# Kernel tuning notes

Measured on AMD Instinct MI355X. Metric: run time of the kernel, lower is better.

The kernel has to match this reference:

```python
import jax, jax.numpy as jnp
import numpy as np

N_WIN = 7    # n_win hardcoded in AR_Attention
TOPK = 4     # topk routing windows
HEADS = 8    # num_heads


def setup_inputs() -> dict:
    key = jax.random.key(0)
    ks = jax.random.split(key, 6)
    B, H, W, C = 4, 56, 56, 256
    s = 0.02
    x = jax.random.normal(ks[0], (B, H, W, C), jnp.float32)
    Wqkv = jax.random.normal(ks[1], (C, 3 * C), jnp.float32) * s  # Linear(dim, 3*dim) (qk_dim=dim)
    bqkv = jnp.zeros((3 * C,), jnp.float32)
    Wo = jax.random.normal(ks[2], (C, C), jnp.float32) * s        # output projection Linear(dim, dim)
    bo = jnp.zeros((C,), jnp.float32)
    lepe_w = jax.random.normal(ks[3], (5, 5, 1, C), jnp.float32) * s  # 5x5 depthwise conv (side_dwconv=5)
    lepe_b = jnp.zeros((C,), jnp.float32)
    return {"x": x, "Wqkv": Wqkv, "bqkv": bqkv, "Wo": Wo, "bo": bo,
            "lepe_w": lepe_w, "lepe_b": lepe_b}


def reference(x, Wqkv, bqkv, Wo, bo, lepe_w, lepe_b):
    B, H, W, C = x.shape
    nw = N_WIN
    h, w = H // nw, W // nw           # region size (8x8)
    p2 = nw * nw                      # number of regions (49)
    hd = C // HEADS                   # head dim
    scale = float(C) ** -0.5          # qk_scale = qk_dim ** -0.5 (qk_dim = dim)

    # region partition: [B,H,W,C] -> [B,p2,h,w,C]
    xr = x.reshape(B, nw, h, nw, w, C).transpose(0, 1, 3, 2, 4, 5).reshape(B, p2, h, w, C)

    qkv = xr @ Wqkv + bqkv            # [B,p2,h,w,3C]
    q, kv = qkv[..., :C], qkv[..., C:]

    q_pix = q.reshape(B, p2, h * w, C)
    kv_pix = kv.reshape(B, p2, h * w, 2 * C)   # kv_downsample_mode='identity'

    # region-level queries/keys via per-window mean pooling
    q_win = q.mean((2, 3))                     # [B,p2,C]
    k_win = kv[..., :C].mean((2, 3))           # [B,p2,C]

    # LEPE: 5x5 depthwise conv on v over the full image grid
    v_img = kv[..., C:].reshape(B, nw, nw, h, w, C).transpose(0, 1, 3, 2, 4, 5).reshape(B, H, W, C)
    lepe = jax.lax.conv_general_dilated(
        v_img, lepe_w, (1, 1), 'SAME',
        dimension_numbers=('NHWC', 'HWIO', 'NHWC'),
        feature_group_count=C) + lepe_b

    # top-k window routing (param_routing=False, hard routing, mul_weight='none')
    r_logit = jnp.einsum('bpc,bqc->bpq', q_win * scale, k_win)  # [B,p2,p2]
    _, r_idx = jax.lax.top_k(r_logit, TOPK)                     # [B,p2,TOPK]

    # gather selected kv windows: [B,p2,TOPK,h*w,2C]
    kv_sel = jax.vmap(lambda kvp, i: kvp[i])(kv_pix, r_idx)

    k_sel = kv_sel[..., :C].reshape(B, p2, TOPK * h * w, HEADS, hd)
    v_sel = kv_sel[..., C:].reshape(B, p2, TOPK * h * w, HEADS, hd)
    qh = q_pix.reshape(B, p2, h * w, HEADS, hd)

    attn = jnp.einsum('bpqnd,bpknd->bpnqk', qh * scale, k_sel)  # [B,p2,heads,hw,TOPK*hw]
    attn = jax.nn.softmax(attn, axis=-1)
    out = jnp.einsum('bpnqk,bpknd->bpqnd', attn, v_sel).reshape(B, p2, h, w, C)

    # windows back to image grid
    out = out.reshape(B, nw, nw, h, w, C).transpose(0, 1, 3, 2, 4, 5).reshape(B, H, W, C)
    out = out + lepe
    return out @ Wo + bo
```

## Files before the change

kernel.cpp:

```cpp
#include <hip/hip_runtime.h>
#include <hip/hip_bf16.h>

#define NPIX 12544

typedef short bf16x8 __attribute__((ext_vector_type(8)));
typedef float f32x4  __attribute__((ext_vector_type(4)));

__device__ __forceinline__ float bf2f(unsigned short u) {
    unsigned int x = ((unsigned int)u) << 16;
    float f; __builtin_memcpy(&f, &x, sizeof(f)); return f;
}
__device__ __forceinline__ unsigned short f2bf(float f) {
    __hip_bfloat16 h = __float2bfloat16(f);
    unsigned short u; __builtin_memcpy(&u, &h, 2); return u;
}
__device__ __forceinline__ void load_lds16(const unsigned short* g, unsigned short* l) {
    __builtin_amdgcn_global_load_lds(
        (const __attribute__((address_space(1))) unsigned int*)g,
        (__attribute__((address_space(3))) unsigned int*)l,
        16, 0, 0);
}

__global__ __launch_bounds__(256) void k_prep(
    const float* __restrict__ X, unsigned short* __restrict__ Xb,
    float* __restrict__ xmean,
    const float* __restrict__ Wqkv, const float* __restrict__ Wo,
    unsigned short* __restrict__ Wtq, unsigned short* __restrict__ Wto)
{
    __shared__ __align__(16) unsigned char sm[64 * 65 * 4];
    const int t = threadIdx.x;
    const int blk = blockIdx.x;
    if (blk < 392) {
        float* part = (float*)sm;
        const int w = blk >> 1, hc = blk & 1;
        const int b = w / 49, p = w % 49;
        const int wi = p / 7, wj = p % 7;
        const int ch0 = hc * 128;
        const int ps = t >> 5, cg = t & 31;
        float4 s = {0.f, 0.f, 0.f, 0.f};
        #pragma unroll
        for (int i = 0; i < 8; i++) {
            int pp = ps * 8 + i;
            int y = wi * 8 + (pp >> 3), x = wj * 8 + (pp & 7);
            int idx = (((b * 56) + y) * 56 + x) * 256 + ch0 + cg * 4;
            float4 v = *reinterpret_cast<const float4*>(X + idx);
            s.x += v.x; s.y += v.y; s.z += v.z; s.w += v.w;
            ushort4 o = { f2bf(v.x), f2bf(v.y), f2bf(v.z), f2bf(v.w) };
            *reinterpret_cast<ushort4*>(Xb + idx) = o;
        }
        *reinterpret_cast<float4*>(part + t * 4) = *reinterpret_cast<float4*>(&s);
        __syncthreads();
        if (t < 32) {
            float4 m = {0.f, 0.f, 0.f, 0.f};
            #pragma unroll
            for (int ps2 = 0; ps2 < 8; ps2++) {
                float4 v = *reinterpret_cast<float4*>(part + (ps2 * 32 + t) * 4);
                m.x += v.x; m.y += v.y; m.z += v.z; m.w += v.w;
            }
            m.x *= (1.f / 64.f); m.y *= (1.f / 64.f);
            m.z *= (1.f / 64.f); m.w *= (1.f / 64.f);
            *reinterpret_cast<float4*>(xmean + w * 256 + ch0 + t * 4) = m;
        }
    } else {
        float* tile = (float*)sm;
        int tb = blk - 392;
        const float* Wsrc; unsigned short* Wdst; int N, kt, nt;
        if (tb < 48) { Wsrc = Wqkv; Wdst = Wtq; N = 768; kt = tb / 12; nt = tb % 12; }
        else { tb -= 48; Wsrc = Wo; Wdst = Wto; N = 256; kt = tb / 4; nt = tb % 4; }
        const int k0 = kt * 64, n0 = nt * 64;
        const int r0 = t >> 6, c = t & 63;
        #pragma unroll
        for (int i = 0; i < 16; i++) {
            int r = i * 4 + r0;
            tile[r * 65 + c] = Wsrc[(size_t)(k0 + r) * N + n0 + c];
        }
        __syncthreads();
        #pragma unroll
        for (int i = 0; i < 16; i++) {
            int n = i * 4 + r0;
            Wdst[(size_t)(n0 + n) * 256 + k0 + c] = f2bf(tile[c * 65 + n]);
        }
    }
}

__global__ __launch_bounds__(256) void k_main1(
    const unsigned short* __restrict__ A,
    const unsigned short* __restrict__ Bt,
    const float* __restrict__ bias,
    unsigned short* __restrict__ O,
    const float* __restrict__ xmean,
    const float* __restrict__ Wqkv,
    float* __restrict__ qwin, float* __restrict__ kwin)
{
    __shared__ __align__(16) unsigned char sm1[16384];
    const int t = threadIdx.x;
    const int blk = blockIdx.x;
    if (blk < 588) {
        unsigned short* As = (unsigned short*)sm1;
        unsigned short* Bs = (unsigned short*)(sm1 + 8192);
        const int m0 = (blk % 98) * 128, n0 = (blk / 98) * 128;
        const int wave = t >> 6, lane = t & 63, quad = lane >> 4, lo = lane & 15;
        const int wm = wave & 1, wn = wave >> 1;
        const int sr = wave * 16 + (lane >> 2);
        const int sc = lane & 3;
        f32x4 acc[4][4];
        #pragma unroll
        for (int i = 0; i < 4; i++)
            #pragma unroll
            for (int j = 0; j < 4; j++) acc[i][j] = (f32x4){0.f, 0.f, 0.f, 0.f};

        for (int kt = 0; kt < 256; kt += 32) {
            __syncthreads();
            #pragma unroll
            for (int j = 0; j < 2; j++) {
                int row = j * 64 + sr;
                int e = sc ^ ((row >> 1) & 3);
                load_lds16(A  + (size_t)(m0 + row) * 256 + kt + e * 8, &As[row * 32 + sc * 8]);
                load_lds16(Bt + (size_t)(n0 + row) * 256 + kt + e * 8, &Bs[row * 32 + sc * 8]);
            }
            __syncthreads();
            bf16x8 af[4], bfr[4];
            #pragma unroll
            for (int mt = 0; mt < 4; mt++) {
                int row = wm * 64 + mt * 16 + lo;
                int c = quad ^ ((row >> 1) & 3);
                af[mt] = *reinterpret_cast<const bf16x8*>(&As[row * 32 + c * 8]);
            }
            #pragma unroll
            for (int nt = 0; nt < 4; nt++) {
                int col = wn * 64 + nt * 16 + lo;
                int c = quad ^ ((col >> 1) & 3);
                bfr[nt] = *reinterpret_cast<const bf16x8*>(&Bs[col * 32 + c * 8]);
            }
            #pragma unroll
            for (int mt = 0; mt < 4; mt++)
                #pragma unroll
                for (int nt = 0; nt < 4; nt++)
                    acc[mt][nt] = __builtin_amdgcn_mfma_f32_16x16x32_bf16(
                        af[mt], bfr[nt], acc[mt][nt], 0, 0, 0);
        }
        float bv[4];
        #pragma unroll
        for (int nt = 0; nt < 4; nt++) bv[nt] = bias[n0 + wn * 64 + nt * 16 + lo];
        #pragma unroll
        for (int mt = 0; mt < 4; mt++)
            #pragma unroll
            for (int nt = 0; nt < 4; nt++) {
                int n = n0 + wn * 64 + nt * 16 + lo;
                #pragma unroll
                for (int r = 0; r < 4; r++) {
                    int m = m0 + wm * 64 + mt * 16 + quad * 4 + r;
                    O[m * 768 + n] = f2bf(acc[mt][nt][r] + bv[nt]);
                }
            }
    } else {
        float* xs = (float*)sm1;
        const int u = blk - 588;
        const int bp = u % 196;
        const int half = u / 196;
        const int c = t;
        xs[c] = xmean[bp * 256 + c];
        __syncthreads();
        const int col = half * 256 + c;
        float a = 0.f;
        for (int k = 0; k < 256; k++) a += xs[k] * Wqkv[k * 768 + col];
        float* outp = half ? kwin : qwin;
        outp[bp * 256 + c] = a + bias[col];
    }
}

__global__ __launch_bounds__(256) void k_main2(
    const float* __restrict__ qwin, const float* __restrict__ kwin,
    int* __restrict__ ridx,
    const unsigned short* __restrict__ QKV,
    const float* __restrict__ lw, const float* __restrict__ lb,
    unsigned short* __restrict__ Olepe)
{
    __shared__ __align__(16) unsigned char sm2[25600];
    const int t = threadIdx.x;
    const int blk = blockIdx.x;
    if (blk < 196) {
        float* part = (float*)sm2;
        float* lg   = (float*)(sm2 + 49 * 4 * 4);
        const int b = blk / 49, p = blk % 49;
        if (t < 196) {
            int d = t >> 2, pr = t & 3;
            const float* qp = &qwin[(b * 49 + p) * 256];
            const float* kp = &kwin[(b * 49 + d) * 256];
            float a = 0.f;
            for (int ch = pr * 64; ch < pr * 64 + 64; ch++) a += qp[ch] * kp[ch];
            part[d * 4 + pr] = a;
        }
        __syncthreads();
        if (t < 49) lg[t] = part[t * 4 + 0] + part[t * 4 + 1] + part[t * 4 + 2] + part[t * 4 + 3];
        __syncthreads();
        if (t == 0) {
            unsigned long long used = 0ull;
            for (int sel = 0; sel < 4; sel++) {
                float best = -1e30f; int bi = 0;
                for (int qq = 0; qq < 49; qq++)
                    if (!((used >> qq) & 1ull) && lg[qq] > best) { best = lg[qq]; bi = qq; }
                used |= (1ull << bi);
                ridx[blk * 4 + sel] = bi;
            }
        }
    } else {
        float* lws = (float*)sm2;
        #pragma unroll
        for (int i = 0; i < 25; i++) lws[i * 256 + t] = lw[i * 256 + t];

        const int pl = t & 7;
        const int cg = t >> 3;
        const int c0 = cg * 8;
        const int gid = (blk - 196) * 8 + pl;
        const int b = gid / 3136, rem = gid % 3136;
        const int y = rem / 56, x = rem % 56;
        __syncthreads();

        float acc[8];
        {
            float4 b0 = *reinterpret_cast<const float4*>(lb + c0);
            float4 b1 = *reinterpret_cast<const float4*>(lb + c0 + 4);
            acc[0] = b0.x; acc[1] = b0.y; acc[2] = b0.z; acc[3] = b0.w;
            acc[4] = b1.x; acc[5] = b1.y; acc[6] = b1.z; acc[7] = b1.w;
        }
        #pragma unroll
        for (int ky = 0; ky < 5; ky++) {
            int yy = y + ky - 2;
            if (yy < 0 || yy >= 56) continue;
            #pragma unroll
            for (int kx = 0; kx < 5; kx++) {
                int xx = x + kx - 2;
                if (xx < 0 || xx >= 56) continue;
                bf16x8 v = *reinterpret_cast<const bf16x8*>(
                    QKV + (((b * 56) + yy) * 56 + xx) * 768 + 512 + c0);
                const float* wrow = &lws[(ky * 5 + kx) * 256 + c0];
                float4 w0 = *reinterpret_cast<const float4*>(wrow);
                float4 w1 = *reinterpret_cast<const float4*>(wrow + 4);
                acc[0] += bf2f((unsigned short)v[0]) * w0.x;
                acc[1] += bf2f((unsigned short)v[1]) * w0.y;
                acc[2] += bf2f((unsigned short)v[2]) * w0.z;
                acc[3] += bf2f((unsigned short)v[3]) * w0.w;
                acc[4] += bf2f((unsigned short)v[4]) * w1.x;
                acc[5] += bf2f((unsigned short)v[5]) * w1.y;
                acc[6] += bf2f((unsigned short)v[6]) * w1.z;
                acc[7] += bf2f((unsigned short)v[7]) * w1.w;
            }
        }
        bf16x8 o;
        #pragma unroll
        for (int j = 0; j < 8; j++) o[j] = (short)f2bf(acc[j]);
        *reinterpret_cast<bf16x8*>(Olepe + (size_t)gid * 256 + c0) = o;
    }
}

__global__ __launch_bounds__(256) void k_attn(
    const unsigned short* __restrict__ QKV,
    const int* __restrict__ ridx,
    const unsigned short* __restrict__ Olepe,
    unsigned short* __restrict__ Osum)
{
    __shared__ __align__(16) unsigned char smem[50688];
    unsigned short* Vt = (unsigned short*)smem;
    unsigned short* Qs = (unsigned short*)(smem + 16896);
    unsigned short* Ks = (unsigned short*)(smem + 22016);
    unsigned short* Ps = (unsigned short*)(smem + 16896);

    const int p = blockIdx.x, head = blockIdx.y, b = blockIdx.z;
    const int t = threadIdx.x;
    const int wi = p / 7, wj = p % 7;
    const int wave = t >> 6, lane = t & 63, quad = lane >> 4, lo = lane & 15;
    const int pix4 = t >> 2, c4 = t & 3;

    {
        int y = wi * 8 + (pix4 >> 3), x = wj * 8 + (pix4 & 7);
        const unsigned short* qp = QKV + (((b * 56) + y) * 56 + x) * 768 + head * 32 + c4 * 8;
        bf16x8 v = *reinterpret_cast<const bf16x8*>(qp);
        int sw = c4 ^ ((pix4 >> 3) & 3);
        *reinterpret_cast<bf16x8*>(&Qs[pix4 * 40 + sw * 8]) = v;
    }
    #pragma unroll
    for (int pass = 0; pass < 4; pass++) {
        int sel = ridx[(b * 49 + p) * 4 + pass];
        int si = sel / 7, sj = sel % 7;
        int y = si * 8 + (pix4 >> 3), x = sj * 8 + (pix4 & 7);
        const unsigned short* base = QKV + (((b * 56) + y) * 56 + x) * 768 + 256 + head * 32;
        bf16x8 kv = *reinterpret_cast<const bf16x8*>(base + c4 * 8);
        bf16x8 vv = *reinterpret_cast<const bf16x8*>(base + 256 + c4 * 8);
        int krow = pass * 64 + pix4;
        int sw = c4 ^ ((krow >> 3) & 3);
        *reinterpret_cast<bf16x8*>(&Ks[krow * 40 + sw * 8]) = kv;
        #pragma unroll
        for (int j = 0; j < 8; j++)
            Vt[(c4 * 8 + j) * 264 + krow] = (unsigned short)vv[j];
    }
    __syncthreads();

    f32x4 sc[16];
    {
        int row = wave * 16 + lo;
        bf16x8 af = *reinterpret_cast<const bf16x8*>(
            &Qs[row * 40 + ((quad ^ ((row >> 3) & 3)) * 8)]);
        f32x4 z = (f32x4){0.f, 0.f, 0.f, 0.f};
        #pragma unroll
        for (int nt = 0; nt < 16; nt++) {
            int key = nt * 16 + lo;
            bf16x8 bfr = *reinterpret_cast<const bf16x8*>(
                &Ks[key * 40 + ((quad ^ ((key >> 3) & 3)) * 8)]);
            sc[nt] = __builtin_amdgcn_mfma_f32_16x16x32_bf16(af, bfr, z, 0, 0, 0);
        }
    }
    float M[4] = {-1e30f, -1e30f, -1e30f, -1e30f};
    #pragma unroll
    for (int nt = 0; nt < 16; nt++)
        #pragma unroll
        for (int r = 0; r < 4; r++) M[r] = fmaxf(M[r], sc[nt][r] * 0.0625f);
    #pragma unroll
    for (int d = 1; d < 16; d <<= 1)
        #pragma unroll
        for (int r = 0; r < 4; r++) M[r] = fmaxf(M[r], __shfl_xor(M[r], d));
    float l[4] = {0.f, 0.f, 0.f, 0.f};
    #pragma unroll
    for (int nt = 0; nt < 16; nt++)
        #pragma unroll
        for (int r = 0; r < 4; r++) {
            float e = __expf(sc[nt][r] * 0.0625f - M[r]);
            sc[nt][r] = e;
            l[r] += e;
        }
    #pragma unroll
    for (int d = 1; d < 16; d <<= 1)
        #pragma unroll
        for (int r = 0; r < 4; r++) l[r] += __shfl_xor(l[r], d);

    __syncthreads();

    unsigned short* myPs = Ps + wave * 16 * 264;
    #pragma unroll
    for (int nt = 0; nt < 16; nt++)
        #pragma unroll
        for (int r = 0; r < 4; r++)
            myPs[(quad * 4 + r) * 264 + nt * 16 + lo] = f2bf(sc[nt][r]);

    f32x4 o0 = (f32x4){0.f, 0.f, 0.f, 0.f}, o1 = o0;
    #pragma unroll
    for (int kt = 0; kt < 8; kt++) {
        bf16x8 pa = *reinterpret_cast<const bf16x8*>(
            &myPs[lo * 264 + kt * 32 + quad * 8]);
        bf16x8 vb0 = *reinterpret_cast<const bf16x8*>(
            &Vt[lo * 264 + kt * 32 + quad * 8]);
        bf16x8 vb1 = *reinterpret_cast<const bf16x8*>(
            &Vt[(16 + lo) * 264 + kt * 32 + quad * 8]);
        o0 = __builtin_amdgcn_mfma_f32_16x16x32_bf16(pa, vb0, o0, 0, 0, 0);
        o1 = __builtin_amdgcn_mfma_f32_16x16x32_bf16(pa, vb1, o1, 0, 0, 0);
    }
    #pragma unroll
    for (int r = 0; r < 4; r++) {
        int q = wave * 16 + quad * 4 + r;
        int y = wi * 8 + (q >> 3), x = wj * 8 + (q & 7);
        size_t base = (size_t)(((b * 56) + y) * 56 + x) * 256 + head * 32;
        const unsigned short* lp = Olepe + base;
        unsigned short* op = Osum + base;
        float inv = 1.0f / l[r];
        op[lo]      = f2bf(o0[r] * inv + bf2f(lp[lo]));
        op[16 + lo] = f2bf(o1[r] * inv + bf2f(lp[16 + lo]));
    }
}

__global__ __launch_bounds__(256) void k_proj(
    const unsigned short* __restrict__ A,
    const unsigned short* __restrict__ Bt,
    const float* __restrict__ bias,
    float* __restrict__ O)
{
    __shared__ unsigned short As[128 * 32];
    __shared__ unsigned short Bs[64 * 32];
    const int t = threadIdx.x;
    const int m0 = blockIdx.x * 128, n0 = blockIdx.y * 64;
    const int wave = t >> 6, lane = t & 63, quad = lane >> 4, lo = lane & 15;
    const int sr = wave * 16 + (lane >> 2);
    const int sc = lane & 3;
    f32x4 acc[2][4];
    #pragma unroll
    for (int i = 0; i < 2; i++)
        #pragma unroll
        for (int j = 0; j < 4; j++) acc[i][j] = (f32x4){0.f, 0.f, 0.f, 0.f};

    for (int kt = 0; kt < 256; kt += 32) {
        __syncthreads();
        #pragma unroll
        for (int j = 0; j < 2; j++) {
            int row = j * 64 + sr;
            int e = sc ^ ((row >> 1) & 3);
            load_lds16(A + (size_t)(m0 + row) * 256 + kt + e * 8, &As[row * 32 + sc * 8]);
        }
        {
            int e = sc ^ ((sr >> 1) & 3);
            load_lds16(Bt + (size_t)(n0 + sr) * 256 + kt + e * 8, &Bs[sr * 32 + sc * 8]);
        }
        __syncthreads();
        bf16x8 af[2], bfr[4];
        #pragma unroll
        for (int mt = 0; mt < 2; mt++) {
            int row = wave * 32 + mt * 16 + lo;
            int c = quad ^ ((row >> 1) & 3);
            af[mt] = *reinterpret_cast<const bf16x8*>(&As[row * 32 + c * 8]);
        }
        #pragma unroll
        for (int nt = 0; nt < 4; nt++) {
            int col = nt * 16 + lo;
            int c = quad ^ ((col >> 1) & 3);
            bfr[nt] = *reinterpret_cast<const bf16x8*>(&Bs[col * 32 + c * 8]);
        }
        #pragma unroll
        for (int mt = 0; mt < 2; mt++)
            #pragma unroll
            for (int nt = 0; nt < 4; nt++)
                acc[mt][nt] = __builtin_amdgcn_mfma_f32_16x16x32_bf16(
                    af[mt], bfr[nt], acc[mt][nt], 0, 0, 0);
    }
    float bv[4];
    #pragma unroll
    for (int nt = 0; nt < 4; nt++) bv[nt] = bias[n0 + nt * 16 + lo];
    #pragma unroll
    for (int mt = 0; mt < 2; mt++)
        #pragma unroll
        for (int nt = 0; nt < 4; nt++) {
            int n = n0 + nt * 16 + lo;
            #pragma unroll
            for (int r = 0; r < 4; r++) {
                int m = m0 + wave * 32 + mt * 16 + quad * 4 + r;
                O[m * 256 + n] = acc[mt][nt][r] + bv[nt];
            }
        }
}

extern "C" void kernel_launch(void* const* d_in, const int* in_sizes, int n_in,
                              void* d_out, int out_size, void* d_ws, size_t ws_size,
                              hipStream_t stream)
{
    const float* x    = (const float*)d_in[0];
    const float* Wqkv = (const float*)d_in[1];
    const float* bqkv = (const float*)d_in[2];
    const float* Wo   = (const float*)d_in[3];
    const float* bo   = (const float*)d_in[4];
    const float* lw   = (const float*)d_in[5];
    const float* lb   = (const float*)d_in[6];
    float* out = (float*)d_out;

    char* ws = (char*)d_ws;
    size_t off = 0;
    unsigned short* qkv   = (unsigned short*)(ws + off); off += (size_t)NPIX * 768 * 2;
    unsigned short* xb    = (unsigned short*)(ws + off); off += (size_t)NPIX * 256 * 2;
    unsigned short* Wtq   = (unsigned short*)(ws + off); off += 768 * 256 * 2;
    unsigned short* Wto   = (unsigned short*)(ws + off); off += 256 * 256 * 2;
    unsigned short* Osum  = (unsigned short*)(ws + off); off += (size_t)NPIX * 256 * 2;
    unsigned short* Olepe = (unsigned short*)(ws + off); off += (size_t)NPIX * 256 * 2;
    float* xmean = (float*)(ws + off); off += 196 * 256 * 4;
    float* qwin  = (float*)(ws + off); off += 196 * 256 * 4;
    float* kwin  = (float*)(ws + off); off += 196 * 256 * 4;
    int*   ridx  = (int*)(ws + off);   off += 196 * 4 * 4;

    k_prep <<<dim3(456),      256, 0, stream>>>(x, xb, xmean, Wqkv, Wo, Wtq, Wto);
    k_main1<<<dim3(980),      256, 0, stream>>>(xb, Wtq, bqkv, qkv, xmean, Wqkv, qwin, kwin);
    k_main2<<<dim3(1764),     256, 0, stream>>>(qwin, kwin, ridx, qkv, lw, lb, Olepe);
    k_attn <<<dim3(49, 8, 4), 256, 0, stream>>>(qkv, ridx, Olepe, Osum);
    k_proj <<<dim3(98, 4),    256, 0, stream>>>(Osum, Wto, bo, out);
}
```

Before: 155.9 us.

## Use LDS transpose reads for P and V operands and vectorize attention output

Replaces the scalar transposed V stores and strided P stores in the attention kernel with packed vector stores into new LDS layouts, then reads MFMA operands with ds_read_b64_tr_b16 transpose loads, software-pipelined one k-step ahead with explicit waitcnts. The output epilogue is staged through LDS and transposed so each lane writes 16-byte vectors and reads the LEPE term with one vector load instead of scalar ones. This targets LDS bank conflicts and scalar global traffic, but adds an extra bf16 rounding before the LEPE add and relies on hand-written asm waitcnt counts.

Measured after the change: 154.5 us. About the same (-0.9%).

```diff
diff --git a/kernel.cpp b/kernel.cpp
--- a/kernel.cpp
+++ b/kernel.cpp
@@ -4,6 +4,7 @@
 #define NPIX 12544
 
 typedef short bf16x8 __attribute__((ext_vector_type(8)));
+typedef short bf16x4 __attribute__((ext_vector_type(4)));
 typedef float f32x4  __attribute__((ext_vector_type(4)));
 
 __device__ __forceinline__ float bf2f(unsigned short u) {
@@ -19,6 +20,16 @@
         (const __attribute__((address_space(1))) unsigned int*)g,
         (__attribute__((address_space(3))) unsigned int*)l,
         16, 0, 0);
+}
+__device__ __forceinline__ unsigned ldsoff(const void* p) {
+    return (unsigned)(unsigned long long)(const __attribute__((address_space(3))) char*)p;
+}
+template<int OFF>
+__device__ __forceinline__ bf16x4 tr16(unsigned addr) {
+    bf16x4 d;
+    asm volatile("ds_read_b64_tr_b16 %0, %1 offset:%c2"
+                 : "=v"(d) : "v"(addr), "i"(OFF));
+    return d;
 }
 
 __global__ __launch_bounds__(256) void k_prep(
@@ -260,11 +271,12 @@
     const unsigned short* __restrict__ Olepe,
     unsigned short* __restrict__ Osum)
 {
-    __shared__ __align__(16) unsigned char smem[50688];
-    unsigned short* Vt = (unsigned short*)smem;
-    unsigned short* Qs = (unsigned short*)(smem + 16896);
-    unsigned short* Ks = (unsigned short*)(smem + 22016);
-    unsigned short* Ps = (unsigned short*)(smem + 16896);
+    __shared__ __align__(16) unsigned char smem[53248];
+    unsigned short* Vs  = (unsigned short*)smem;
+    unsigned short* Qs  = (unsigned short*)(smem + 16384);
+    unsigned short* Ks  = (unsigned short*)(smem + 21504);
+    unsigned short* PST = (unsigned short*)(smem + 16384);
+    unsigned short* OsT = (unsigned short*)(smem + 49152);
 
     const int p = blockIdx.x, head = blockIdx.y, b = blockIdx.z;
     const int t = threadIdx.x;
@@ -290,9 +302,8 @@
         int krow = pass * 64 + pix4;
         int sw = c4 ^ ((krow >> 3) & 3);
         *reinterpret_cast<bf16x8*>(&Ks[krow * 40 + sw * 8]) = kv;
-        #pragma unroll
-        for (int j = 0; j < 8; j++)
-            Vt[(c4 * 8 + j) * 264 + krow] = (unsigned short)vv[j];
+        *reinterpret_cast<bf16x8*>(
+            &Vs[(krow >> 2) * 128 + (c4 >> 1) * 64 + (krow & 3) * 16 + (c4 & 1) * 8]) = vv;
     }
     __syncthreads();
 
@@ -335,35 +346,84 @@
 
     __syncthreads();
 
-    unsigned short* myPs = Ps + wave * 16 * 264;
-    #pragma unroll
-    for (int nt = 0; nt < 16; nt++)
-        #pragma unroll
-        for (int r = 0; r < 4; r++)
-            myPs[(quad * 4 + r) * 264 + nt * 16 + lo] = f2bf(sc[nt][r]);
-
+    unsigned short* myP = PST + wave * 4096;
+    #pragma unroll
+    for (int nt = 0; nt < 16; nt++) {
+        ushort4 pk = { f2bf(sc[nt][0]), f2bf(sc[nt][1]),
+                       f2bf(sc[nt][2]), f2bf(sc[nt][3]) };
+        *reinterpret_cast<ushort4*>(&myP[(nt * 16 + lo) * 16 + quad * 4]) = pk;
+    }
+    const unsigned paddr = ldsoff(myP) + quad * 256 + lo * 8;
+    const unsigned vaddr = ldsoff(Vs)  + quad * 512 + lo * 8;
+    asm volatile("s_waitcnt lgkmcnt(0)" ::: "memory");
+    __builtin_amdgcn_sched_barrier(0);
+
+    bf16x4 ra0, ra1, rw00, rw01, rw10, rw11;
+    ra0  = tr16<0>(paddr);
+    ra1  = tr16<128>(paddr);
+    rw00 = tr16<0>(vaddr);
+    rw01 = tr16<256>(vaddr);
+    rw10 = tr16<128>(vaddr);
+    rw11 = tr16<384>(vaddr);
     f32x4 o0 = (f32x4){0.f, 0.f, 0.f, 0.f}, o1 = o0;
     #pragma unroll
     for (int kt = 0; kt < 8; kt++) {
-        bf16x8 pa = *reinterpret_cast<const bf16x8*>(
-            &myPs[lo * 264 + kt * 32 + quad * 8]);
-        bf16x8 vb0 = *reinterpret_cast<const bf16x8*>(
-            &Vt[lo * 264 + kt * 32 + quad * 8]);
-        bf16x8 vb1 = *reinterpret_cast<const bf16x8*>(
-            &Vt[(16 + lo) * 264 + kt * 32 + quad * 8]);
+        bf16x4 na0, na1, nw00, nw01, nw10, nw11;
+        if (kt < 7) {
+            unsigned pn = paddr + (kt + 1) * 1024;
+            unsigned vn = vaddr + (kt + 1) * 2048;
+            na0  = tr16<0>(pn);
+            na1  = tr16<128>(pn);
+            nw00 = tr16<0>(vn);
+            nw01 = tr16<256>(vn);
+            nw10 = tr16<128>(vn);
+            nw11 = tr16<384>(vn);
+            asm volatile("s_waitcnt lgkmcnt(6)" ::: "memory");
+        } else {
+            asm volatile("s_waitcnt lgkmcnt(0)" ::: "memory");
+        }
+        __builtin_amdgcn_sched_barrier(0);
+        bf16x8 pa, vb0, vb1;
+        #pragma unroll
+        for (int j = 0; j < 4; j++) {
+            pa[j]  = ra0[j];  pa[4 + j]  = ra1[j];
+            vb0[j] = rw00[j]; vb0[4 + j] = rw01[j];
+            vb1[j] = rw10[j]; vb1[4 + j] = rw11[j];
+        }
         o0 = __builtin_amdgcn_mfma_f32_16x16x32_bf16(pa, vb0, o0, 0, 0, 0);
         o1 = __builtin_amdgcn_mfma_f32_16x16x32_bf16(pa, vb1, o1, 0, 0, 0);
-    }
-    #pragma unroll
-    for (int r = 0; r < 4; r++) {
-        int q = wave * 16 + quad * 4 + r;
+        if (kt < 7) { ra0 = na0; ra1 = na1; rw00 = nw00; rw01 = nw01; rw10 = nw10; rw11 = nw11; }
+    }
+
+    {
+        unsigned short* ow = OsT + wave * 512;
+        float i0 = 1.f / l[0], i1 = 1.f / l[1], i2 = 1.f / l[2], i3 = 1.f / l[3];
+        ushort4 p0 = { f2bf(o0[0] * i0), f2bf(o0[1] * i1),
+                       f2bf(o0[2] * i2), f2bf(o0[3] * i3) };
+        ushort4 p1 = { f2bf(o1[0] * i0), f2bf(o1[1] * i1),
+                       f2bf(o1[2] * i2), f2bf(o1[3] * i3) };
+        *reinterpret_cast<ushort4*>(&ow[lo * 16 + quad * 4]) = p0;
+        *reinterpret_cast<ushort4*>(&ow[(16 + lo) * 16 + quad * 4]) = p1;
+    }
+    const unsigned oaddr = ldsoff(OsT) + wave * 1024 + quad * 256 + lo * 8;
+    asm volatile("s_waitcnt lgkmcnt(0)" ::: "memory");
+    __builtin_amdgcn_sched_barrier(0);
+    bf16x4 e0 = tr16<0>(oaddr);
+    bf16x4 e1 = tr16<128>(oaddr);
+    asm volatile("s_waitcnt lgkmcnt(0)" ::: "memory");
+    __builtin_amdgcn_sched_barrier(0);
+    {
+        int q = wave * 16 + lo;
         int y = wi * 8 + (q >> 3), x = wj * 8 + (q & 7);
-        size_t base = (size_t)(((b * 56) + y) * 56 + x) * 256 + head * 32;
-        const unsigned short* lp = Olepe + base;
-        unsigned short* op = Osum + base;
-        float inv = 1.0f / l[r];
-        op[lo]      = f2bf(o0[r] * inv + bf2f(lp[lo]));
-        op[16 + lo] = f2bf(o1[r] * inv + bf2f(lp[16 + lo]));
+        size_t gbase = (size_t)(((b * 56) + y) * 56 + x) * 256 + head * 32 + quad * 8;
+        bf16x8 lp = *reinterpret_cast<const bf16x8*>(Olepe + gbase);
+        bf16x8 oo;
+        #pragma unroll
+        for (int j = 0; j < 4; j++) {
+            oo[j]     = (short)f2bf(bf2f((unsigned short)e0[j]) + bf2f((unsigned short)lp[j]));
+            oo[4 + j] = (short)f2bf(bf2f((unsigned short)e1[j]) + bf2f((unsigned short)lp[4 + j]));
+        }
+        *reinterpret_cast<bf16x8*>(Osum + gbase) = oo;
     }
 }
 
```
